# Kernel tuning notes

Hardware: AMD Instinct MI355X
Metric: run time of the kernel (lower is better)

Reference implementation:

```python
import jax, jax.numpy as jnp
import numpy as np

BATCH, TIMESTEPS, DIM, OUT = 64, 512, 1024, 1024


def setup_inputs() -> dict:
    key = jax.random.key(0)
    k1, k2, k3, k4, k5, k6 = jax.random.split(key, 6)
    # glorot-normal-ish scales for params
    def glorot(k, shape):
        fan_in, fan_out = shape[0], shape[-1]
        std = (2.0 / (fan_in + fan_out)) ** 0.5
        return jax.random.normal(k, shape, dtype=jnp.float32) * std
    return {
        "inputs": jax.random.normal(k1, (BATCH, TIMESTEPS, DIM), dtype=jnp.float32),
        "prev_state": jax.random.normal(k2, (BATCH, OUT), dtype=jnp.float32),
        "Wa": glorot(k3, (OUT, OUT)),
        "Ua": glorot(k4, (DIM, OUT)),
        "Va": glorot(k5, (OUT, 1)),
        "Ba": glorot(k6, (1, OUT)),
    }


def reference(inputs, prev_state, Wa, Ua, Va, Ba):
    # WaS: [B, 1, OUT] broadcast over timesteps
    WaS = jnp.einsum("bo,op->bp", prev_state, Wa)[:, None, :]
    # UaH: [B, T, OUT]
    UaH = jnp.einsum("btd,do->bto", inputs, Ua)
    scores = jnp.tanh(UaH + WaS + Ba)            # [B, T, OUT]
    scores = jax.nn.relu(scores @ Va)            # [B, T, 1]
    sm = jax.nn.softmax(scores, axis=1)          # softmax over timesteps
    context_vector = jnp.sum(inputs * sm, axis=1)  # [B, DIM]
    return context_vector
```

## Files before the change

### kernel.cpp

```cpp
#include <hip/hip_runtime.h>


typedef _Float16 h8 __attribute__((ext_vector_type(8)));
typedef float f16v __attribute__((ext_vector_type(16)));

__device__ __forceinline__ float tanh_fast(float x) {
    float e = __expf(2.0f * x);
    return 1.0f - 2.0f * __builtin_amdgcn_rcpf(e + 1.0f);
}

__global__ __launch_bounds__(256) void k_pack_ua(const float* __restrict__ Ua,
                                                 _Float16* __restrict__ B16) {
    int t = blockIdx.x * 256 + threadIdx.x;
    int nn = t & 31, kg = (t >> 5) & 1, ks = (t >> 6) & 63, nt = t >> 12;
    int n = (nt << 5) + nn;
    int kbase = (ks << 4) + (kg << 3);
    h8 v;
#pragma unroll
    for (int j = 0; j < 8; ++j) v[j] = (_Float16)Ua[(size_t)(kbase + j) * 1024 + n];
    *(h8*)(B16 + ((size_t)t << 3)) = v;
}

__global__ __launch_bounds__(256) void k_pack_a(const float* __restrict__ inputs,
                                                _Float16* __restrict__ A16) {
    const int bx = blockIdx.x, t = threadIdx.x;
    const int rl = t >> 3, oc0 = t & 7;
    const float4* src = (const float4*)(inputs + (((size_t)bx * 32 + rl) << 10));
    h8* dst = (h8*)A16 + ((size_t)bx << 12) + rl;
#pragma unroll
    for (int i = 0; i < 16; ++i) {
        int o = oc0 + (i << 3);
        float4 v0 = src[o * 2], v1 = src[o * 2 + 1];
        h8 ov = { (_Float16)v0.x, (_Float16)v0.y, (_Float16)v0.z, (_Float16)v0.w,
                  (_Float16)v1.x, (_Float16)v1.y, (_Float16)v1.z, (_Float16)v1.w };
        dst[((o >> 1) << 6) + ((o & 1) << 5)] = ov;
    }
}

__global__ __launch_bounds__(256) void k_was_part(const float* __restrict__ ps,
                                                  const float* __restrict__ Wa,
                                                  float* __restrict__ part) {
    int ic = blockIdx.x >> 2, psl = blockIdx.x & 3;
    int tid = threadIdx.x, wv = tid >> 6, lane = tid & 63;
    int p4 = psl * 64 + lane;
    const float4* Wa4 = (const float4*)Wa;
    float4* part4 = (float4*)part;
#pragma unroll 1
    for (int c = 0; c < 4; ++c) {
        int o0 = ic * 128 + c * 32;
        float4 w[32];
#pragma unroll
        for (int o = 0; o < 32; ++o) w[o] = Wa4[(size_t)(o0 + o) * 256 + p4];
#pragma unroll 1
        for (int bb = 0; bb < 16; ++bb) {
            int b = wv * 16 + bb;
            const float* psb = ps + b * 1024 + o0;
            size_t oidx = (size_t)((ic << 6) + b) * 256 + p4;
            float4 a;
            if (c == 0) { a.x = a.y = a.z = a.w = 0.f; }
            else        { a = part4[oidx]; }
#pragma unroll
            for (int o = 0; o < 32; ++o) {
                float s = psb[o];
                a.x += s * w[o].x; a.y += s * w[o].y;
                a.z += s * w[o].z; a.w += s * w[o].w;
            }
            part4[oidx] = a;
        }
    }
}

__global__ __launch_bounds__(256) void k_was_reduce(const float* __restrict__ part,
                                                    const float* __restrict__ Ba,
                                                    float* __restrict__ wsWaS) {
    int b = blockIdx.x, tid = threadIdx.x;
    const float4* p4 = (const float4*)part;
    float4 acc = ((const float4*)Ba)[tid];
#pragma unroll
    for (int ic = 0; ic < 8; ++ic) {
        float4 v = p4[((ic << 6) + b) * 256 + tid];
        acc.x += v.x; acc.y += v.y; acc.z += v.z; acc.w += v.w;
    }
    ((float4*)wsWaS)[b * 256 + tid] = acc;
}

__global__ __launch_bounds__(256, 2) void k_fused_gemm(
    const _Float16* __restrict__ A16, const _Float16* __restrict__ B16,
    const float* __restrict__ wsWaS, const float* __restrict__ Va,
    float* __restrict__ scores)
{
    __shared__ float scoreSh[64];
    const int tid = threadIdx.x;
    const int lane = tid & 63, wv = tid >> 6;
    const int l31 = lane & 31, lhi = lane >> 5;
    const int r0 = blockIdx.x * 64;
    const int rb0 = blockIdx.x * 2;
    const int b = r0 >> 9;

    if (tid < 64) scoreSh[tid] = 0.0f;
    __syncthreads();

    const h8* A8 = (const h8*)A16;
    const h8* B8 = (const h8*)B16;
    const h8* aBase = A8 + ((size_t)rb0 << 12) + lane;

    for (int pass = 0; pass < 2; ++pass) {
        const int ntb = (pass << 4) + (wv << 2);
        const h8* bBase = B8 + ((size_t)ntb << 12) + lane;

        f16v acc[2][4];
#pragma unroll
        for (int rt = 0; rt < 2; ++rt)
#pragma unroll
            for (int ct = 0; ct < 4; ++ct)
#pragma unroll
                for (int e = 0; e < 16; ++e) acc[rt][ct][e] = 0.0f;

        h8 af[4][2], bf[2][4];
#pragma unroll
        for (int p = 0; p < 4; ++p)
#pragma unroll
            for (int rt = 0; rt < 2; ++rt) af[p][rt] = aBase[rt * 4096 + p * 64];
#pragma unroll
        for (int ct = 0; ct < 4; ++ct) bf[0][ct] = bBase[ct * 4096];

#pragma unroll 4
        for (int ks = 0; ks < 64; ++ks) {
            const int cur = ks & 1, nxt = cur ^ 1, ra = ks & 3;
            h8 a0 = af[ra][0], a1 = af[ra][1];
            if (ks < 60) {
                const int o = (ks + 4) << 6;
                af[ra][0] = aBase[o];
                af[ra][1] = aBase[4096 + o];
            }
            if (ks < 63) {
                const int o = (ks + 1) << 6;
#pragma unroll
                for (int ct = 0; ct < 4; ++ct) bf[nxt][ct] = bBase[ct * 4096 + o];
            }
#pragma unroll
            for (int ct = 0; ct < 4; ++ct) {
                acc[0][ct] = __builtin_amdgcn_mfma_f32_32x32x16_f16(a0, bf[cur][ct], acc[0][ct], 0, 0, 0);
                acc[1][ct] = __builtin_amdgcn_mfma_f32_32x32x16_f16(a1, bf[cur][ct], acc[1][ct], 0, 0, 0);
            }
        }

        float wsv[4], vav[4];
#pragma unroll
        for (int ct = 0; ct < 4; ++ct) {
            int n = (ntb + ct) << 5 | l31;
            wsv[ct] = wsWaS[b * 1024 + n];
            vav[ct] = Va[n];
        }
#pragma unroll
        for (int rt = 0; rt < 2; ++rt) {
#pragma unroll
            for (int i = 0; i < 16; ++i) {
                float s = 0.0f;
#pragma unroll
                for (int ct = 0; ct < 4; ++ct)
                    s += tanh_fast(acc[rt][ct][i] + wsv[ct]) * vav[ct];
                s += __shfl_xor(s, 1);
                s += __shfl_xor(s, 2);
                s += __shfl_xor(s, 4);
                s += __shfl_xor(s, 8);
                s += __shfl_xor(s, 16);
                if (l31 == 0) {
                    int row = rt * 32 + (i & 3) + ((i >> 2) << 3) + (lhi << 2);
                    atomicAdd(&scoreSh[row], s);
                }
            }
        }
    }
    __syncthreads();
    if (tid < 64) scores[r0 + tid] = fmaxf(scoreSh[tid], 0.0f);
}

__global__ __launch_bounds__(256) void k_softmax(const float* __restrict__ scores,
                                                 float* __restrict__ sm) {
    int b = blockIdx.x, tid = threadIdx.x;
    __shared__ float red[256];
    const float* sb = scores + b * 512;
    float s0 = sb[tid], s1 = sb[tid + 256];
    red[tid] = fmaxf(s0, s1);
    __syncthreads();
    for (int st = 128; st > 0; st >>= 1) {
        if (tid < st) red[tid] = fmaxf(red[tid], red[tid + st]);
        __syncthreads();
    }
    float m = red[0];
    __syncthreads();
    float e0 = __expf(s0 - m), e1 = __expf(s1 - m);
    red[tid] = e0 + e1;
    __syncthreads();
    for (int st = 128; st > 0; st >>= 1) {
        if (tid < st) red[tid] += red[tid + st];
        __syncthreads();
    }
    float inv = 1.0f / red[0];
    sm[b * 512 + tid] = e0 * inv;
    sm[b * 512 + 256 + tid] = e1 * inv;
}

__global__ __launch_bounds__(256) void k_ctx(const _Float16* __restrict__ A16,
                                             const float* __restrict__ sm,
                                             float* __restrict__ out) {
    const int bx = blockIdx.x, b = blockIdx.y;
    const int tid = threadIdx.x, wv = tid >> 6, lane = tid & 63;
    const int l31 = lane & 31, lhi = lane >> 5;
    const h8* A8 = (const h8*)A16;
    const int ksl = bx * 4 + wv;
    float facc[8];
#pragma unroll
    for (int j = 0; j < 8; ++j) facc[j] = 0.0f;
    const float* smb = sm + b * 512;
#pragma unroll 4
    for (int rbl = 0; rbl < 16; ++rbl) {
        h8 x = A8[(((size_t)(b * 16 + rbl) << 6) + ksl) * 64 + lane];
        float wgt = smb[rbl * 32 + l31];
#pragma unroll
        for (int j = 0; j < 8; ++j) facc[j] += wgt * (float)x[j];
    }
#pragma unroll
    for (int m = 1; m < 32; m <<= 1)
#pragma unroll
        for (int j = 0; j < 8; ++j) facc[j] += __shfl_xor(facc[j], m);
    if (l31 == 0) {
        int oct = bx * 8 + wv * 2 + lhi;
        float* o = out + b * 1024 + oct * 8;
#pragma unroll
        for (int j = 0; j < 8; ++j) o[j] = facc[j];
    }
}

extern "C" void kernel_launch(void* const* d_in, const int* in_sizes, int n_in,
                              void* d_out, int out_size, void* d_ws, size_t ws_size,
                              hipStream_t stream) {
    const float* inputs = (const float*)d_in[0];
    const float* prev   = (const float*)d_in[1];
    const float* Wa     = (const float*)d_in[2];
    const float* Ua     = (const float*)d_in[3];
    const float* Va     = (const float*)d_in[4];
    const float* Ba     = (const float*)d_in[5];
    float* out = (float*)d_out;

    char* ws = (char*)d_ws;
    _Float16* A16   = (_Float16*)(ws);
    _Float16* B16   = (_Float16*)(ws + (64u << 20));
    float* wasPart  = (float*)(ws + (66u << 20));
    float* wsWaS    = (float*)(ws + (68u << 20));
    float* scores   = (float*)(ws + (68u << 20) + (256u << 10));
    float* sm       = (float*)(ws + (68u << 20) + (384u << 10));

    hipLaunchKernelGGL(k_pack_ua,    dim3(512),    dim3(256), 0, stream, Ua, B16);
    hipLaunchKernelGGL(k_pack_a,     dim3(1024),   dim3(256), 0, stream, inputs, A16);
    hipLaunchKernelGGL(k_was_part,   dim3(32),     dim3(256), 0, stream, prev, Wa, wasPart);
    hipLaunchKernelGGL(k_was_reduce, dim3(64),     dim3(256), 0, stream, wasPart, Ba, wsWaS);
    hipLaunchKernelGGL(k_fused_gemm, dim3(512),    dim3(256), 0, stream, A16, B16, wsWaS, Va, scores);
    hipLaunchKernelGGL(k_softmax,    dim3(64),     dim3(256), 0, stream, scores, sm);
    hipLaunchKernelGGL(k_ctx,        dim3(16, 64), dim3(256), 0, stream, A16, sm, out);
}
```

Baseline: 367.3 us.

## Stage pack_a through LDS, fuse WaS kernels, simplify GEMM A prefetch

k_pack_a now loads input rows through padded shared memory with coalesced float4 reads before writing the fp16 MFMA layout, instead of reading strided float4 pairs directly. The two-kernel WaS computation (partial sums plus reduce) is merged into one kernel that keeps prev_state rows in LDS and streams Wa columns, dropping one launch and the partial buffer. The GEMM's 4-deep A register prefetch becomes a 2-stage double buffer matching B, which lowers register pressure but hides less load latency.

```diff
diff --git a/kernel.cpp b/kernel.cpp
--- a/kernel.cpp
+++ b/kernel.cpp
@@ -21,67 +21,61 @@
     *(h8*)(B16 + ((size_t)t << 3)) = v;
 }
 
+#define PA_STR 65
 __global__ __launch_bounds__(256) void k_pack_a(const float* __restrict__ inputs,
                                                 _Float16* __restrict__ A16) {
+    __shared__ float4 T[32 * PA_STR];
     const int bx = blockIdx.x, t = threadIdx.x;
-    const int rl = t >> 3, oc0 = t & 7;
-    const float4* src = (const float4*)(inputs + (((size_t)bx * 32 + rl) << 10));
-    h8* dst = (h8*)A16 + ((size_t)bx << 12) + rl;
-#pragma unroll
-    for (int i = 0; i < 16; ++i) {
-        int o = oc0 + (i << 3);
-        float4 v0 = src[o * 2], v1 = src[o * 2 + 1];
-        h8 ov = { (_Float16)v0.x, (_Float16)v0.y, (_Float16)v0.z, (_Float16)v0.w,
-                  (_Float16)v1.x, (_Float16)v1.y, (_Float16)v1.z, (_Float16)v1.w };
-        dst[((o >> 1) << 6) + ((o & 1) << 5)] = ov;
-    }
-}
-
-__global__ __launch_bounds__(256) void k_was_part(const float* __restrict__ ps,
-                                                  const float* __restrict__ Wa,
-                                                  float* __restrict__ part) {
-    int ic = blockIdx.x >> 2, psl = blockIdx.x & 3;
-    int tid = threadIdx.x, wv = tid >> 6, lane = tid & 63;
-    int p4 = psl * 64 + lane;
-    const float4* Wa4 = (const float4*)Wa;
-    float4* part4 = (float4*)part;
+    const size_t r0 = (size_t)bx * 32;
+    h8* outBase = (h8*)A16 + ((size_t)bx << 12);
 #pragma unroll 1
-    for (int c = 0; c < 4; ++c) {
-        int o0 = ic * 128 + c * 32;
-        float4 w[32];
-#pragma unroll
-        for (int o = 0; o < 32; ++o) w[o] = Wa4[(size_t)(o0 + o) * 256 + p4];
-#pragma unroll 1
-        for (int bb = 0; bb < 16; ++bb) {
-            int b = wv * 16 + bb;
-            const float* psb = ps + b * 1024 + o0;
-            size_t oidx = (size_t)((ic << 6) + b) * 256 + p4;
-            float4 a;
-            if (c == 0) { a.x = a.y = a.z = a.w = 0.f; }
-            else        { a = part4[oidx]; }
-#pragma unroll
-            for (int o = 0; o < 32; ++o) {
-                float s = psb[o];
-                a.x += s * w[o].x; a.y += s * w[o].y;
-                a.z += s * w[o].z; a.w += s * w[o].w;
-            }
-            part4[oidx] = a;
-        }
-    }
-}
-
-__global__ __launch_bounds__(256) void k_was_reduce(const float* __restrict__ part,
-                                                    const float* __restrict__ Ba,
-                                                    float* __restrict__ wsWaS) {
-    int b = blockIdx.x, tid = threadIdx.x;
-    const float4* p4 = (const float4*)part;
-    float4 acc = ((const float4*)Ba)[tid];
-#pragma unroll
-    for (int ic = 0; ic < 8; ++ic) {
-        float4 v = p4[((ic << 6) + b) * 256 + tid];
-        acc.x += v.x; acc.y += v.y; acc.z += v.z; acc.w += v.w;
-    }
-    ((float4*)wsWaS)[b * 256 + tid] = acc;
+    for (int kc = 0; kc < 4; ++kc) {
+        if (kc) __syncthreads();
+#pragma unroll
+        for (int i = 0; i < 8; ++i) {
+            int p = (i << 8) + t;
+            int row = p >> 6, c4 = p & 63;
+            T[row * PA_STR + c4] =
+                ((const float4*)(inputs + (r0 + row) * 1024 + (kc << 8)))[c4];
+        }
+        __syncthreads();
+#pragma unroll
+        for (int i = 0; i < 4; ++i) {
+            int p = (i << 8) + t;
+            int ks8 = p >> 6, l = p & 63;
+            int row = l & 31, k8 = l >> 5;
+            float4 v0 = T[row * PA_STR + (ks8 << 2) + (k8 << 1)];
+            float4 v1 = T[row * PA_STR + (ks8 << 2) + (k8 << 1) + 1];
+            outBase[(((kc << 4) + ks8) << 6) + l] =
+                (h8){ (_Float16)v0.x, (_Float16)v0.y, (_Float16)v0.z, (_Float16)v0.w,
+                      (_Float16)v1.x, (_Float16)v1.y, (_Float16)v1.z, (_Float16)v1.w };
+        }
+    }
+}
+
+__global__ __launch_bounds__(256) void k_was(const float* __restrict__ ps,
+                                             const float* __restrict__ Wa,
+                                             const float* __restrict__ Ba,
+                                             float* __restrict__ wsWaS) {
+    __shared__ float psL[8][1024];
+    const int bg = blockIdx.x >> 3, cg = blockIdx.x & 7;
+    const int t = threadIdx.x;
+#pragma unroll
+    for (int i = 0; i < 8; ++i)
+        ((float4*)psL[i])[t] = ((const float4*)(ps + (size_t)(bg * 8 + i) * 1024))[t];
+    __syncthreads();
+    const int c4 = (cg << 5) + (t & 31);
+    const int br = t >> 5;
+    const float4* WaC = (const float4*)Wa + c4;
+    const float* prow = psL[br];
+    float4 acc = ((const float4*)Ba)[c4];
+#pragma unroll 8
+    for (int o = 0; o < 1024; ++o) {
+        float s = prow[o];
+        float4 w = WaC[(size_t)o * 256];
+        acc.x += s * w.x; acc.y += s * w.y; acc.z += s * w.z; acc.w += s * w.w;
+    }
+    ((float4*)wsWaS)[(size_t)(bg * 8 + br) * 256 + c4] = acc;
 }
 
 __global__ __launch_bounds__(256, 2) void k_fused_gemm(
@@ -116,33 +110,28 @@
 #pragma unroll
                 for (int e = 0; e < 16; ++e) acc[rt][ct][e] = 0.0f;
 
-        h8 af[4][2], bf[2][4];
-#pragma unroll
-        for (int p = 0; p < 4; ++p)
-#pragma unroll
-            for (int rt = 0; rt < 2; ++rt) af[p][rt] = aBase[rt * 4096 + p * 64];
+        h8 af[2][2], bf[2][4];
+#pragma unroll
+        for (int rt = 0; rt < 2; ++rt) af[0][rt] = aBase[rt * 4096];
 #pragma unroll
         for (int ct = 0; ct < 4; ++ct) bf[0][ct] = bBase[ct * 4096];
 
 #pragma unroll 4
         for (int ks = 0; ks < 64; ++ks) {
-            const int cur = ks & 1, nxt = cur ^ 1, ra = ks & 3;
-            h8 a0 = af[ra][0], a1 = af[ra][1];
-            if (ks < 60) {
-                const int o = (ks + 4) << 6;
-                af[ra][0] = aBase[o];
-                af[ra][1] = aBase[4096 + o];
-            }
+            const int cur = ks & 1, nxt = cur ^ 1;
             if (ks < 63) {
                 const int o = (ks + 1) << 6;
 #pragma unroll
+                for (int rt = 0; rt < 2; ++rt) af[nxt][rt] = aBase[rt * 4096 + o];
+#pragma unroll
                 for (int ct = 0; ct < 4; ++ct) bf[nxt][ct] = bBase[ct * 4096 + o];
             }
 #pragma unroll
-            for (int ct = 0; ct < 4; ++ct) {
-                acc[0][ct] = __builtin_amdgcn_mfma_f32_32x32x16_f16(a0, bf[cur][ct], acc[0][ct], 0, 0, 0);
-                acc[1][ct] = __builtin_amdgcn_mfma_f32_32x32x16_f16(a1, bf[cur][ct], acc[1][ct], 0, 0, 0);
-            }
+            for (int rt = 0; rt < 2; ++rt)
+#pragma unroll
+                for (int ct = 0; ct < 4; ++ct)
+                    acc[rt][ct] = __builtin_amdgcn_mfma_f32_32x32x16_f16(
+                        af[cur][rt], bf[cur][ct], acc[rt][ct], 0, 0, 0);
         }
 
         float wsv[4], vav[4];
@@ -245,17 +234,15 @@
     float* out = (float*)d_out;
 
     char* ws = (char*)d_ws;
-    _Float16* A16   = (_Float16*)(ws);
-    _Float16* B16   = (_Float16*)(ws + (64u << 20));
-    float* wasPart  = (float*)(ws + (66u << 20));
-    float* wsWaS    = (float*)(ws + (68u << 20));
-    float* scores   = (float*)(ws + (68u << 20) + (256u << 10));
-    float* sm       = (float*)(ws + (68u << 20) + (384u << 10));
+    _Float16* A16 = (_Float16*)(ws);
+    _Float16* B16 = (_Float16*)(ws + (64u << 20));
+    float* wsWaS  = (float*)(ws + (66u << 20));
+    float* scores = (float*)(ws + (66u << 20) + (256u << 10));
+    float* sm     = (float*)(ws + (66u << 20) + (384u << 10));
 
     hipLaunchKernelGGL(k_pack_ua,    dim3(512),    dim3(256), 0, stream, Ua, B16);
     hipLaunchKernelGGL(k_pack_a,     dim3(1024),   dim3(256), 0, stream, inputs, A16);
-    hipLaunchKernelGGL(k_was_part,   dim3(32),     dim3(256), 0, stream, prev, Wa, wasPart);
-    hipLaunchKernelGGL(k_was_reduce, dim3(64),     dim3(256), 0, stream, wasPart, Ba, wsWaS);
+    hipLaunchKernelGGL(k_was,        dim3(64),     dim3(256), 0, stream, prev, Wa, Ba, wsWaS);
     hipLaunchKernelGGL(k_fused_gemm, dim3(512),    dim3(256), 0, stream, A16, B16, wsWaS, Va, scores);
     hipLaunchKernelGGL(k_softmax,    dim3(64),     dim3(256), 0, stream, scores, sm);
     hipLaunchKernelGGL(k_ctx,        dim3(16, 64), dim3(256), 0, stream, A16, sm, out);
```

After: 397.1 us. 8.1% more time.
